# Kernel optimization log

Hardware: AMD Instinct MI355X
Metric: run time of the kernel (lower is better)

## Reference

```python
import jax, jax.numpy as jnp
import numpy as np

B, S, D, H = 1, 4096, 1024, 16
HD = D // H  # head_dim = 64
NEG = -1e9


def _rotate_half(x):
    x1, x2 = jnp.split(x, 2, axis=-1)
    return jnp.concatenate([-x2, x1], axis=-1)


def _apply_rope(x, cos, sin):
    # x: [b, s, h, hd]; cos/sin: [s, hd] -> broadcast over batch and heads
    c = cos[None, :, None, :]
    s = sin[None, :, None, :]
    return x * c + _rotate_half(x) * s


def setup_inputs() -> dict:
    key = jax.random.key(0)
    kx, kq, ko = jax.random.split(key, 3)
    x = jax.random.normal(kx, (B, S, D), dtype=jnp.float32)
    # causal additive mask (finite large-negative for safe grads)
    i = jnp.arange(S)
    attn_mask = jnp.where(i[None, :] > i[:, None], NEG, 0.0).astype(jnp.float32)[None, None]
    # standard RoPE tables
    inv_freq = 1.0 / (10000.0 ** (np.arange(0, HD, 2, dtype=np.float32) / HD))
    ang = np.arange(S, dtype=np.float32)[:, None] * inv_freq[None, :]  # [S, HD/2]
    ang = np.concatenate([ang, ang], axis=-1)  # [S, HD]
    rope_cos = jnp.asarray(np.cos(ang))
    rope_sin = jnp.asarray(np.sin(ang))
    W_qkv = jax.random.normal(kq, (D, 3 * D), dtype=jnp.float32) * (D ** -0.5)
    W_out = jax.random.normal(ko, (D, D), dtype=jnp.float32) * (D ** -0.5)
    return {"x": x, "attn_mask": attn_mask, "rope_cos": rope_cos,
            "rope_sin": rope_sin, "W_qkv": W_qkv, "W_out": W_out}


def reference(x, attn_mask, rope_cos, rope_sin, W_qkv, W_out):
    b, s, d = x.shape
    qkv = x @ W_qkv                              # [b, s, 3d]
    q, k, v = jnp.split(qkv, 3, axis=-1)
    q = q.reshape(b, s, H, HD)
    k = k.reshape(b, s, H, HD)
    v = v.reshape(b, s, H, HD)
    q = _apply_rope(q, rope_cos, rope_sin)
    k = _apply_rope(k, rope_cos, rope_sin)
    att = jnp.einsum('bqhd,bkhd->bhqk', q, k) / jnp.sqrt(jnp.float32(HD))
    att = att + attn_mask                        # additive mask broadcast [b,h,s,s]
    att = jax.nn.softmax(att, axis=-1)
    out = jnp.einsum('bhqk,bkhd->bqhd', att, v).reshape(b, s, d)
    return out @ W_out
```

## Files before the change

kernel.cpp:

```cpp
#include <hip/hip_runtime.h>


typedef __attribute__((ext_vector_type(8)))  __bf16 bf16x8;
typedef __attribute__((ext_vector_type(4)))  float  f32x4;
typedef __attribute__((ext_vector_type(16))) float  f32x16;
typedef __attribute__((ext_vector_type(8)))  unsigned short ushort8;
typedef __attribute__((ext_vector_type(4)))  unsigned int   u32x4;

#define MFMA16(a,b,c) __builtin_amdgcn_mfma_f32_16x16x32_bf16((a),(b),(c),0,0,0)
#define MFMA32(a,b,c) __builtin_amdgcn_mfma_f32_32x32x16_bf16((a),(b),(c),0,0,0)

static __device__ __forceinline__ unsigned short f2bf(float f) {
  unsigned int u = __builtin_bit_cast(unsigned int, f);
  u = (u + 0x7FFFu + ((u >> 16) & 1u)) >> 16;
  return (unsigned short)u;
}
static __device__ __forceinline__ float bf2f(unsigned short u) {
  return __builtin_bit_cast(float, (unsigned int)u << 16);
}
static __device__ __forceinline__ unsigned int cvtpk(float a, float b) {
  unsigned int r;
  asm("v_cvt_pk_bf16_f32 %0, %1, %2" : "=v"(r) : "v"(a), "v"(b));
  return r;
}
static __device__ __forceinline__ void plswap(unsigned int& a, unsigned int& b) {
#if __has_builtin(__builtin_amdgcn_permlane32_swap)
  auto r = __builtin_amdgcn_permlane32_swap(a, b, false, false);
  a = r[0]; b = r[1];
#else
  unsigned int xa = (unsigned int)__shfl_xor((int)a, 32);
  unsigned int xb = (unsigned int)__shfl_xor((int)b, 32);
  int lane = __builtin_amdgcn_mbcnt_hi(~0u, __builtin_amdgcn_mbcnt_lo(~0u, 0));
  bool hi = lane >= 32;
  a = hi ? xb : a;
  b = hi ? b : xa;
#endif
}
static __device__ __forceinline__ void gll16(const unsigned short* gp, const unsigned short* lp) {
  unsigned int m0v = __builtin_amdgcn_readfirstlane((unsigned int)(unsigned long long)(uintptr_t)lp);
  asm volatile("s_mov_b32 m0, %0\n\tglobal_load_lds_dwordx4 %1, off"
               :: "s"(m0v), "v"(gp) : "memory");
}
static __device__ __forceinline__ void wait_dma() {
  asm volatile("s_waitcnt vmcnt(0)" ::: "memory");
}

__global__ __launch_bounds__(256) void prep_a(const float* __restrict__ x,
                                              const float* __restrict__ W_qkv,
                                              const float* __restrict__ W_out,
                                              unsigned short* __restrict__ xbf,
                                              unsigned short* __restrict__ WqkvT,
                                              unsigned short* __restrict__ WoutT) {
  __shared__ float t[32][33];
  int b = blockIdx.x, tid = threadIdx.x;
  if (b < 4096) {
    int i = (b * 256 + tid) * 4;
    float4 v = *reinterpret_cast<const float4*>(x + i);
    ushort4 u;
    u.x = f2bf(v.x); u.y = f2bf(v.y); u.z = f2bf(v.z); u.w = f2bf(v.w);
    *reinterpret_cast<ushort4*>(xbf + i) = u;
    return;
  }
  const float* W; unsigned short* WT; int R, C, cx, ry;
  if (b < 4096 + 3072) {
    int idx = b - 4096; W = W_qkv; WT = WqkvT; R = 1024; C = 3072;
    cx = idx % 96; ry = idx / 96;
  } else {
    int idx = b - 7168; W = W_out; WT = WoutT; R = 1024; C = 1024;
    cx = idx % 32; ry = idx / 32;
  }
  int c0 = cx * 32, r0 = ry * 32;
  int tx = tid & 31, ty = tid >> 5;
#pragma unroll
  for (int i = 0; i < 32; i += 8)
    t[ty + i][tx] = W[(size_t)(r0 + ty + i) * C + c0 + tx];
  __syncthreads();
#pragma unroll
  for (int i = 0; i < 32; i += 8)
    WT[(size_t)(c0 + ty + i) * R + r0 + tx] = f2bf(t[tx][ty + i]);
}

template <typename OutT>
__global__ __launch_bounds__(256) void gemm_lds(const unsigned short* __restrict__ A,
                                                const unsigned short* __restrict__ BT,
                                                OutT* __restrict__ C, int M, int N, int K) {
  __shared__ __align__(16) unsigned short As[128 * 32];
  __shared__ __align__(16) unsigned short Bs[128 * 32];
  int tid = threadIdx.x;
  int lane = tid & 63, w = tid >> 6;
  int wr = w >> 1, wc = w & 1;
  int row0 = blockIdx.y * 128, col0 = blockIdx.x * 128;
  int lr = lane & 15, lk = lane >> 4;
  int slk = (lk ^ ((lr >> 1) & 3)) * 8;
  f32x4 acc[4][4] = {};
  for (int k0 = 0; k0 < K; k0 += 32) {
#pragma unroll
    for (int i = 0; i < 2; ++i) {
      int c = i * 256 + tid;
      int r = c >> 2, cc = c & 3;
      int ccs = cc ^ ((r >> 1) & 3);
      gll16(A  + (size_t)(row0 + r) * K + k0 + ccs * 8, &As[i * 2048 + w * 512]);
      gll16(BT + (size_t)(col0 + r) * K + k0 + ccs * 8, &Bs[i * 2048 + w * 512]);
    }
    wait_dma();
    __syncthreads();
    bf16x8 a[4], b[4];
#pragma unroll
    for (int m = 0; m < 4; m++)
      a[m] = *reinterpret_cast<const bf16x8*>(&As[(wr * 64 + m * 16 + lr) * 32 + slk]);
#pragma unroll
    for (int n = 0; n < 4; n++)
      b[n] = *reinterpret_cast<const bf16x8*>(&Bs[(wc * 64 + n * 16 + lr) * 32 + slk]);
#pragma unroll
    for (int m = 0; m < 4; m++)
#pragma unroll
      for (int n = 0; n < 4; n++)
        acc[m][n] = MFMA16(a[m], b[n], acc[m][n]);
    __syncthreads();
  }
#pragma unroll
  for (int m = 0; m < 4; m++)
#pragma unroll
    for (int n = 0; n < 4; n++)
#pragma unroll
      for (int r = 0; r < 4; r++) {
        size_t off = (size_t)(row0 + wr * 64 + m * 16 + lk * 4 + r) * N + col0 + wc * 64 + n * 16 + lr;
        if constexpr (sizeof(OutT) == 2) C[off] = f2bf(acc[m][n][r]);
        else                             C[off] = acc[m][n][r];
      }
}

__global__ __launch_bounds__(256) void prep_b(const unsigned short* __restrict__ qkv,
                                              const float* __restrict__ cosb,
                                              const float* __restrict__ sinb,
                                              unsigned short* __restrict__ Q,
                                              unsigned short* __restrict__ K,
                                              unsigned short* __restrict__ VF) {
  __shared__ unsigned short tile[32][68];
  int b = blockIdx.x, tid = threadIdx.x;
  if (b < 2048) {
    const float QSCALE = 0.125f * 1.4426950408889634f;
    int idx = b * 256 + tid;
    int c = idx & 7, s = (idx >> 3) & 4095, h = idx >> 15;
    int d0 = c * 8;
    int base = s * 3072 + h * 64;
    ushort8 qv  = *reinterpret_cast<const ushort8*>(qkv + base + d0);
    ushort8 qv2 = *reinterpret_cast<const ushort8*>(qkv + base + (d0 ^ 32));
    ushort8 kv  = *reinterpret_cast<const ushort8*>(qkv + base + 1024 + d0);
    ushort8 kv2 = *reinterpret_cast<const ushort8*>(qkv + base + 1024 + (d0 ^ 32));
    float sign = (d0 < 32) ? -1.f : 1.f;
    const float4* cp = reinterpret_cast<const float4*>(cosb + s * 64 + d0);
    const float4* sp = reinterpret_cast<const float4*>(sinb + s * 64 + d0);
    float4 c0 = cp[0], c1 = cp[1], s0 = sp[0], s1 = sp[1];
    float co[8] = {c0.x, c0.y, c0.z, c0.w, c1.x, c1.y, c1.z, c1.w};
    float si[8] = {s0.x, s0.y, s0.z, s0.w, s1.x, s1.y, s1.z, s1.w};
    ushort8 qo, ko;
#pragma unroll
    for (int j = 0; j < 8; ++j) {
      float q = bf2f(qv[j]), q2 = bf2f(qv2[j]);
      float k = bf2f(kv[j]), k2 = bf2f(kv2[j]);
      qo[j] = f2bf((q * co[j] + sign * q2 * si[j]) * QSCALE);
      ko[j] = f2bf(k * co[j] + sign * k2 * si[j]);
    }
    *reinterpret_cast<ushort8*>(Q + (size_t)h * 262144 + (size_t)s * 64 + d0) = qo;
    int tt = s >> 5, ql = s & 31, lo = (d0 >> 3) & 1, f = d0 >> 4;
    size_t koff = (size_t)h * 262144 + (size_t)tt * 2048 + (size_t)f * 512
                + (size_t)(lo * 32 + ql) * 8;
    *reinterpret_cast<ushort8*>(K + koff) = ko;
    return;
  }
  int vb = b - 2048;
  int t = vb & 127, h = vb >> 7;
  {
    int r = tid >> 3, c8 = (tid & 7) * 8;
    *reinterpret_cast<ushort8*>(&tile[r][c8]) =
        *reinterpret_cast<const ushort8*>(qkv + (size_t)(t * 32 + r) * 3072 + 2048 + h * 64 + c8);
  }
  __syncthreads();
  int f = tid >> 6, lane = tid & 63;
  int ql = lane & 31, lo = lane >> 5;
  int sb = (f & 1) * 16 + lo * 8;
  int d  = (f >> 1) * 32 + ql;
  ushort8 v;
#pragma unroll
  for (int j = 0; j < 8; ++j) v[j] = tile[sb + j][d];
  *reinterpret_cast<ushort8*>(VF + (size_t)h * 262144 + (size_t)t * 2048
                              + (size_t)f * 512 + (size_t)lane * 8) = v;
}

__global__ __launch_bounds__(256) void flash_attn32(const unsigned short* __restrict__ Q,
                                                    const unsigned short* __restrict__ Kf,
                                                    const unsigned short* __restrict__ Vf,
                                                    unsigned short* __restrict__ O) {
  const int S = 4096;
  __shared__ __align__(16) unsigned short sbuf[2][4][2048];
  int flat = blockIdx.x;
  int xcd = flat & 7;
  int v = flat >> 3;
  int h2 = v >> 6, a = (v >> 5) & 1, u = v & 31;
  int h = xcd * 2 + h2;
  int base = a ? (2 * u) : (126 - 2 * u);
  int tid = threadIdx.x;
  int lane = tid & 63, w = tid >> 6;
  int qm = w & 1, pp = w >> 1;
  int ql = lane & 31, lo = lane >> 5;
  const unsigned short* Qh  = Q  + (size_t)h * S * 64;
  const unsigned short* KfH = Kf + (size_t)h * S * 64;
  const unsigned short* VfH = Vf + (size_t)h * S * 64;

  const unsigned short* img_src = (w & 1) ? VfH : KfH;
  int img_dt = w >> 1;
  auto stage = [&](int nb, int win) {
    int t = 2 * win + img_dt;
    const unsigned short* src = img_src + (size_t)t * 2048;
    const unsigned short* dst = &sbuf[nb][w][0];
#pragma unroll
    for (int j = 0; j < 4; ++j)
      gll16(src + j * 512 + lane * 8, dst + j * 512);
  };

  int qt = base + qm;
  int q0 = qt * 32;
  int nwin = base / 2 + 1;
  bf16x8 qf[4];
#pragma unroll
  for (int f = 0; f < 4; ++f)
    qf[f] = *reinterpret_cast<const bf16x8*>(Qh + (q0 + ql) * 64 + f * 16 + lo * 8);
  f32x16 oT0 = {}, oT1 = {};
  float l = 0.f;

  stage(0, 0);
  wait_dma();
  __syncthreads();
  int cb = 0;
  for (int win = 0; win < nwin; ++win) {
    if (win + 1 < nwin) stage(cb ^ 1, win + 1);
    int t = 2 * win + pp;
    if (t <= qt) {
      const unsigned short* kb = &sbuf[cb][2 * pp][0];
      const unsigned short* vb = &sbuf[cb][2 * pp + 1][0];
      bf16x8 k0 = *reinterpret_cast<const bf16x8*>(kb + 0 * 512 + lane * 8);
      bf16x8 k1 = *reinterpret_cast<const bf16x8*>(kb + 1 * 512 + lane * 8);
      bf16x8 k2 = *reinterpret_cast<const bf16x8*>(kb + 2 * 512 + lane * 8);
      bf16x8 k3 = *reinterpret_cast<const bf16x8*>(kb + 3 * 512 + lane * 8);
      f32x16 p = {};
      __builtin_amdgcn_s_setprio(1);
      p = MFMA32(k0, qf[0], p);
      p = MFMA32(k1, qf[1], p);
      p = MFMA32(k2, qf[2], p);
      p = MFMA32(k3, qf[3], p);
      __builtin_amdgcn_s_setprio(0);
      bf16x8 v00 = *reinterpret_cast<const bf16x8*>(vb + 0 * 512 + lane * 8);
      bf16x8 v01 = *reinterpret_cast<const bf16x8*>(vb + 1 * 512 + lane * 8);
      bf16x8 v10 = *reinterpret_cast<const bf16x8*>(vb + 2 * 512 + lane * 8);
      bf16x8 v11 = *reinterpret_cast<const bf16x8*>(vb + 3 * 512 + lane * 8);
      if (t == qt) {
#pragma unroll
        for (int r = 0; r < 16; ++r) {
          int kvr = (r & 3) + 8 * (r >> 2) + 4 * lo;
          if (kvr > ql) p[r] = -1e9f;
        }
      }
#pragma unroll
      for (int r = 0; r < 16; ++r) p[r] = __builtin_amdgcn_exp2f(p[r]);
      {
        float s0 = (p[0] + p[1])   + (p[2] + p[3]);
        float s1 = (p[4] + p[5])   + (p[6] + p[7]);
        float s2 = (p[8] + p[9])   + (p[10] + p[11]);
        float s3 = (p[12] + p[13]) + (p[14] + p[15]);
        l += (s0 + s1) + (s2 + s3);
      }
      unsigned int A0 = cvtpk(p[0],  p[1]),  A1 = cvtpk(p[2],  p[3]);
      unsigned int B0 = cvtpk(p[4],  p[5]),  B1 = cvtpk(p[6],  p[7]);
      plswap(A0, B0); plswap(A1, B1);
      u32x4 w0 = {A0, A1, B0, B1};
      bf16x8 P0 = __builtin_bit_cast(bf16x8, w0);
      unsigned int C0 = cvtpk(p[8],  p[9]),  C1 = cvtpk(p[10], p[11]);
      unsigned int D0 = cvtpk(p[12], p[13]), D1 = cvtpk(p[14], p[15]);
      plswap(C0, D0); plswap(C1, D1);
      u32x4 w1 = {C0, C1, D0, D1};
      bf16x8 P1 = __builtin_bit_cast(bf16x8, w1);
      __builtin_amdgcn_s_setprio(1);
      oT0 = MFMA32(v00, P0, oT0);
      oT1 = MFMA32(v10, P0, oT1);
      oT0 = MFMA32(v01, P1, oT0);
      oT1 = MFMA32(v11, P1, oT1);
      __builtin_amdgcn_s_setprio(0);
    }
    wait_dma();
    __syncthreads();
    cb ^= 1;
  }

  float* fm = reinterpret_cast<float*>(&sbuf[0][0][0]);
  float* lm = fm + 2 * 64 * 33;
  if (pp == 1) {
    float* dst = fm + (qm * 64 + lane) * 33;
#pragma unroll
    for (int r = 0; r < 16; ++r) { dst[r] = oT0[r]; dst[16 + r] = oT1[r]; }
    lm[qm * 64 + lane] = l;
  }
  __syncthreads();
  if (pp == 0) {
    const float* src = fm + (qm * 64 + lane) * 33;
#pragma unroll
    for (int r = 0; r < 16; ++r) {
      oT0[r] += src[r];
      oT1[r] += src[16 + r];
    }
    l += lm[qm * 64 + lane];
    l += __shfl_xor(l, 32);
    float rl = 1.0f / l;
    size_t obase = (size_t)(q0 + ql) * 1024 + h * 64;
#pragma unroll
    for (int r = 0; r < 16; ++r) {
      int d = (r & 3) + 8 * (r >> 2) + 4 * lo;
      O[obase + d]      = f2bf(oT0[r] * rl);
      O[obase + 32 + d] = f2bf(oT1[r] * rl);
    }
  }
}

extern "C" void kernel_launch(void* const* d_in, const int* in_sizes, int n_in,
                              void* d_out, int out_size, void* d_ws, size_t ws_size,
                              hipStream_t stream) {
  const float* x        = (const float*)d_in[0];
  const float* rope_cos = (const float*)d_in[2];
  const float* rope_sin = (const float*)d_in[3];
  const float* W_qkv    = (const float*)d_in[4];
  const float* W_out    = (const float*)d_in[5];
  float* out = (float*)d_out;

  char* ws = (char*)d_ws;
  const size_t MB = 1u << 20;
  unsigned short* xbf   = (unsigned short*)(ws + 0 * MB);
  unsigned short* WqkvT = (unsigned short*)(ws + 8 * MB);
  unsigned short* WoutT = (unsigned short*)(ws + 14 * MB);
  unsigned short* qkv   = (unsigned short*)(ws + 16 * MB);
  unsigned short* Qb    = (unsigned short*)(ws + 40 * MB);
  unsigned short* Kfb   = (unsigned short*)(ws + 48 * MB);
  unsigned short* Vfb   = (unsigned short*)(ws + 56 * MB);
  unsigned short* Ob    = (unsigned short*)(ws + 64 * MB);

  prep_a<<<8192, 256, 0, stream>>>(x, W_qkv, W_out, xbf, WqkvT, WoutT);

  gemm_lds<unsigned short><<<dim3(3072 / 128, 4096 / 128), 256, 0, stream>>>(
      xbf, WqkvT, qkv, 4096, 3072, 1024);

  prep_b<<<4096, 256, 0, stream>>>(qkv, rope_cos, rope_sin, Qb, Kfb, Vfb);

  flash_attn32<<<1024, 256, 0, stream>>>(Qb, Kfb, Vfb, Ob);

  gemm_lds<float><<<dim3(1024 / 128, 4096 / 128), 256, 0, stream>>>(
      Ob, WoutT, out, 4096, 1024, 1024);
}
```

Baseline: 140.9 us.

## Use 512-thread flash blocks covering four query tiles sharing staged K/V

The attention kernel now launches 512 blocks of 512 threads, each covering four consecutive 32-row query tiles, with eight waves sharing each staged K/V window. This halves the number of times each K/V tile is loaded into LDS per head, and each wave issues half as many DMA loads. The final cross-wave reduction now runs in two rounds through the same LDS scratch. The GEMM also precomputes its swizzled source and destination pointers and issues the four LDS DMA loads from a single asm block. The risks are lower occupancy, coarser causal load balancing across blocks, and extra barriers in the epilogue.

Measured after the change: 135.0 us. 1.04x faster.

```diff
diff --git a/kernel.cpp b/kernel.cpp
--- a/kernel.cpp
+++ b/kernel.cpp
@@ -40,6 +40,22 @@
   unsigned int m0v = __builtin_amdgcn_readfirstlane((unsigned int)(unsigned long long)(uintptr_t)lp);
   asm volatile("s_mov_b32 m0, %0\n\tglobal_load_lds_dwordx4 %1, off"
                :: "s"(m0v), "v"(gp) : "memory");
+}
+static __device__ __forceinline__ void gll16x4(const unsigned short* g0, const unsigned short* l0,
+                                               const unsigned short* g1, const unsigned short* l1,
+                                               const unsigned short* g2, const unsigned short* l2,
+                                               const unsigned short* g3, const unsigned short* l3) {
+  unsigned int m0a = __builtin_amdgcn_readfirstlane((unsigned int)(unsigned long long)(uintptr_t)l0);
+  unsigned int m0b = __builtin_amdgcn_readfirstlane((unsigned int)(unsigned long long)(uintptr_t)l1);
+  unsigned int m0c = __builtin_amdgcn_readfirstlane((unsigned int)(unsigned long long)(uintptr_t)l2);
+  unsigned int m0d = __builtin_amdgcn_readfirstlane((unsigned int)(unsigned long long)(uintptr_t)l3);
+  asm volatile(
+      "s_mov_b32 m0, %0\n\tglobal_load_lds_dwordx4 %4, off\n\t"
+      "s_mov_b32 m0, %1\n\tglobal_load_lds_dwordx4 %5, off\n\t"
+      "s_mov_b32 m0, %2\n\tglobal_load_lds_dwordx4 %6, off\n\t"
+      "s_mov_b32 m0, %3\n\tglobal_load_lds_dwordx4 %7, off"
+      :: "s"(m0a), "s"(m0b), "s"(m0c), "s"(m0d),
+         "v"(g0), "v"(g1), "v"(g2), "v"(g3) : "memory");
 }
 static __device__ __forceinline__ void wait_dma() {
   asm volatile("s_waitcnt vmcnt(0)" ::: "memory");
@@ -92,16 +108,19 @@
   int row0 = blockIdx.y * 128, col0 = blockIdx.x * 128;
   int lr = lane & 15, lk = lane >> 4;
   int slk = (lk ^ ((lr >> 1) & 3)) * 8;
+  int c0i = tid,        r0i = c0i >> 2, cs0 = ((c0i & 3) ^ ((r0i >> 1) & 3)) * 8;
+  int c1i = 256 + tid,  r1i = c1i >> 2, cs1 = ((c1i & 3) ^ ((r1i >> 1) & 3)) * 8;
+  const unsigned short* dA0 = &As[w * 512];
+  const unsigned short* dB0 = &Bs[w * 512];
+  const unsigned short* dA1 = &As[2048 + w * 512];
+  const unsigned short* dB1 = &Bs[2048 + w * 512];
+  const unsigned short* sA0 = A  + (size_t)(row0 + r0i) * K + cs0;
+  const unsigned short* sB0 = BT + (size_t)(col0 + r0i) * K + cs0;
+  const unsigned short* sA1 = A  + (size_t)(row0 + r1i) * K + cs1;
+  const unsigned short* sB1 = BT + (size_t)(col0 + r1i) * K + cs1;
   f32x4 acc[4][4] = {};
   for (int k0 = 0; k0 < K; k0 += 32) {
-#pragma unroll
-    for (int i = 0; i < 2; ++i) {
-      int c = i * 256 + tid;
-      int r = c >> 2, cc = c & 3;
-      int ccs = cc ^ ((r >> 1) & 3);
-      gll16(A  + (size_t)(row0 + r) * K + k0 + ccs * 8, &As[i * 2048 + w * 512]);
-      gll16(BT + (size_t)(col0 + r) * K + k0 + ccs * 8, &Bs[i * 2048 + w * 512]);
-    }
+    gll16x4(sA0 + k0, dA0, sB0 + k0, dB0, sA1 + k0, dA1, sB1 + k0, dB1);
     wait_dma();
     __syncthreads();
     bf16x8 a[4], b[4];
@@ -188,7 +207,7 @@
                               + (size_t)f * 512 + (size_t)lane * 8) = v;
 }
 
-__global__ __launch_bounds__(256) void flash_attn32(const unsigned short* __restrict__ Q,
+__global__ __launch_bounds__(512) void flash_attn4q(const unsigned short* __restrict__ Q,
                                                     const unsigned short* __restrict__ Kf,
                                                     const unsigned short* __restrict__ Vf,
                                                     unsigned short* __restrict__ O) {
@@ -197,31 +216,32 @@
   int flat = blockIdx.x;
   int xcd = flat & 7;
   int v = flat >> 3;
-  int h2 = v >> 6, a = (v >> 5) & 1, u = v & 31;
+  int h2 = v >> 5, gslot = v & 31;
   int h = xcd * 2 + h2;
-  int base = a ? (2 * u) : (126 - 2 * u);
+  int g = h2 ? (31 - gslot) : gslot;
+  int base4 = 4 * g;
+  int nwin = 2 * g + 2;
   int tid = threadIdx.x;
   int lane = tid & 63, w = tid >> 6;
-  int qm = w & 1, pp = w >> 1;
+  int qm = w >> 1, pp = w & 1;
+  int img = w >> 1, half = w & 1;
   int ql = lane & 31, lo = lane >> 5;
   const unsigned short* Qh  = Q  + (size_t)h * S * 64;
   const unsigned short* KfH = Kf + (size_t)h * S * 64;
   const unsigned short* VfH = Vf + (size_t)h * S * 64;
-
-  const unsigned short* img_src = (w & 1) ? VfH : KfH;
-  int img_dt = w >> 1;
+  const unsigned short* img_src = (img & 1) ? VfH : KfH;
+  int img_dt = img >> 1;
+
   auto stage = [&](int nb, int win) {
     int t = 2 * win + img_dt;
-    const unsigned short* src = img_src + (size_t)t * 2048;
-    const unsigned short* dst = &sbuf[nb][w][0];
-#pragma unroll
-    for (int j = 0; j < 4; ++j)
-      gll16(src + j * 512 + lane * 8, dst + j * 512);
+    const unsigned short* src = img_src + (size_t)t * 2048 + half * 1024 + lane * 8;
+    const unsigned short* dst = &sbuf[nb][img][half * 1024];
+    gll16(src, dst);
+    gll16(src + 512, dst + 512);
   };
 
-  int qt = base + qm;
+  int qt = base4 + qm;
   int q0 = qt * 32;
-  int nwin = base / 2 + 1;
   bf16x8 qf[4];
 #pragma unroll
   for (int f = 0; f < 4; ++f)
@@ -294,29 +314,33 @@
 
   float* fm = reinterpret_cast<float*>(&sbuf[0][0][0]);
   float* lm = fm + 2 * 64 * 33;
-  if (pp == 1) {
-    float* dst = fm + (qm * 64 + lane) * 33;
-#pragma unroll
-    for (int r = 0; r < 16; ++r) { dst[r] = oT0[r]; dst[16 + r] = oT1[r]; }
-    lm[qm * 64 + lane] = l;
-  }
-  __syncthreads();
-  if (pp == 0) {
-    const float* src = fm + (qm * 64 + lane) * 33;
-#pragma unroll
-    for (int r = 0; r < 16; ++r) {
-      oT0[r] += src[r];
-      oT1[r] += src[16 + r];
+#pragma unroll
+  for (int sub = 0; sub < 2; ++sub) {
+    __syncthreads();
+    if ((qm >> 1) == sub && pp == 1) {
+      float* dst = fm + ((qm & 1) * 64 + lane) * 33;
+#pragma unroll
+      for (int r = 0; r < 16; ++r) { dst[r] = oT0[r]; dst[16 + r] = oT1[r]; }
+      lm[(qm & 1) * 64 + lane] = l;
     }
-    l += lm[qm * 64 + lane];
-    l += __shfl_xor(l, 32);
-    float rl = 1.0f / l;
-    size_t obase = (size_t)(q0 + ql) * 1024 + h * 64;
-#pragma unroll
-    for (int r = 0; r < 16; ++r) {
-      int d = (r & 3) + 8 * (r >> 2) + 4 * lo;
-      O[obase + d]      = f2bf(oT0[r] * rl);
-      O[obase + 32 + d] = f2bf(oT1[r] * rl);
+    __syncthreads();
+    if ((qm >> 1) == sub && pp == 0) {
+      const float* src = fm + ((qm & 1) * 64 + lane) * 33;
+      float ll = l + lm[(qm & 1) * 64 + lane];
+#pragma unroll
+      for (int r = 0; r < 16; ++r) {
+        oT0[r] += src[r];
+        oT1[r] += src[16 + r];
+      }
+      ll += __shfl_xor(ll, 32);
+      float rl = 1.0f / ll;
+      size_t obase = (size_t)(q0 + ql) * 1024 + h * 64;
+#pragma unroll
+      for (int r = 0; r < 16; ++r) {
+        int d = (r & 3) + 8 * (r >> 2) + 4 * lo;
+        O[obase + d]      = f2bf(oT0[r] * rl);
+        O[obase + 32 + d] = f2bf(oT1[r] * rl);
+      }
     }
   }
 }
@@ -349,7 +373,7 @@
 
   prep_b<<<4096, 256, 0, stream>>>(qkv, rope_cos, rope_sin, Qb, Kfb, Vfb);
 
-  flash_attn32<<<1024, 256, 0, stream>>>(Qb, Kfb, Vfb, Ob);
+  flash_attn4q<<<512, 512, 0, stream>>>(Qb, Kfb, Vfb, Ob);
 
   gemm_lds<float><<<dim3(1024 / 128, 4096 / 128), 256, 0, stream>>>(
       Ob, WoutT, out, 4096, 1024, 1024);
```
